# Optimization experiments

Measured on AMD Instinct MI355X. Metric: run time of the kernel, lower is better.

## Reference

```python
import jax, jax.numpy as jnp
import numpy as np

B, S, D, H = 2, 2048, 1024, 16
HD = D // H  # 64


def setup_inputs() -> dict:
    key = jax.random.key(0)
    ks = jax.random.split(key, 9)
    sd = 1.0 / np.sqrt(D)  # torch Linear default init scale (uniform, but normal ok for ref)
    return {
        "x": jax.random.normal(ks[0], (B, S, D), dtype=jnp.float32),
        # torch Linear weight is [out, in]; stack per head -> [H, HD, D]
        "Wq": jax.random.normal(ks[1], (H, HD, D), dtype=jnp.float32) * sd,
        "bq": jax.random.normal(ks[2], (H, HD), dtype=jnp.float32) * sd,
        "Wk": jax.random.normal(ks[3], (H, HD, D), dtype=jnp.float32) * sd,
        "bk": jax.random.normal(ks[4], (H, HD), dtype=jnp.float32) * sd,
        "Wv": jax.random.normal(ks[5], (H, HD, D), dtype=jnp.float32) * sd,
        "bv": jax.random.normal(ks[6], (H, HD), dtype=jnp.float32) * sd,
        "Wp": jax.random.normal(ks[7], (D, D), dtype=jnp.float32) * sd,
        "bp": jax.random.normal(ks[8], (D,), dtype=jnp.float32) * sd,
    }


def reference(x, Wq, bq, Wk, bk, Wv, bv, Wp, bp):
    # Per-head QKV projections, batched over heads: [B,S,D] x [H,HD,D] -> [B,H,S,HD]
    q = jnp.einsum("bsd,hed->bhse", x, Wq) + bq[None, :, None, :]
    k = jnp.einsum("bsd,hed->bhse", x, Wk) + bk[None, :, None, :]
    v = jnp.einsum("bsd,hed->bhse", x, Wv) + bv[None, :, None, :]
    scale = 1.0 / np.sqrt(HD)
    scores = jnp.einsum("bhse,bhte->bhst", q, k) * scale  # [B,H,S,S]
    attn = jax.nn.softmax(scores, axis=-1)
    out = jnp.einsum("bhst,bhte->bhse", attn, v)  # [B,H,S,HD]
    # concat heads along last dim (head-major order matches torch.cat over heads)
    out = out.transpose(0, 2, 1, 3).reshape(x.shape[0], x.shape[1], -1)  # [B,S,D]
    return out @ Wp.T + bp
```

## Files before the change

kernel.cpp:

```cpp
#include <hip/hip_runtime.h>
#include <hip/hip_bf16.h>
#include <stdint.h>

#define B_  2
#define S_  2048
#define D_  1024
#define H_  16
#define HD_ 64
#define M_  (B_*S_)
#define BH_ (B_*H_)

typedef __bf16 bf16;
typedef bf16  bf16x8 __attribute__((ext_vector_type(8)));
typedef bf16  bf16x4 __attribute__((ext_vector_type(4)));
typedef bf16  bf16x2 __attribute__((ext_vector_type(2)));
typedef float f32x4  __attribute__((ext_vector_type(4)));

#define SCALE_LOG2E 0.18033688011112042f
#define MFIX_LOG2E  23.083120654223415f

__device__ __forceinline__ f32x4 mfma16(bf16x8 a, bf16x8 b, f32x4 c) {
    return __builtin_amdgcn_mfma_f32_16x16x32_bf16(a, b, c, 0, 0, 0);
}
__device__ __forceinline__ float fexp2(float x) {
    return __builtin_amdgcn_exp2f(x);
}

__device__ __forceinline__ void gload_lds16(const bf16* g, bf16* l) {
    auto* gp = reinterpret_cast<__attribute__((address_space(1))) uint32_t*>(
        reinterpret_cast<uintptr_t>(const_cast<bf16*>(g)));
    auto* lp = reinterpret_cast<__attribute__((address_space(3))) uint32_t*>(
        reinterpret_cast<uintptr_t>(l));
    __builtin_amdgcn_global_load_lds(gp, lp, 16, 0, 0);
}

__global__ __launch_bounds__(256) void k_convert(
        const float* __restrict__ x,
        const float* __restrict__ wq, const float* __restrict__ wk,
        const float* __restrict__ wv, const float* __restrict__ wp,
        bf16* __restrict__ xb,
        bf16* __restrict__ wqb, bf16* __restrict__ wkb,
        bf16* __restrict__ wvb, bf16* __restrict__ wpb) {
    const int y = blockIdx.y;
    const float* src = (y == 0) ? x : (y == 1) ? wq : (y == 2) ? wk
                     : (y == 3) ? wv : wp;
    bf16* dst        = (y == 0) ? xb : (y == 1) ? wqb : (y == 2) ? wkb
                     : (y == 3) ? wvb : wpb;
    const int reps = (y == 0) ? 4 : 1;
    const int idx = blockIdx.x * 256 + threadIdx.x;
    for (int rep = 0; rep < reps; ++rep) {
        const size_t e = (size_t)rep * (1u << 20) + (size_t)idx * 4;
        const float4 f = *(const float4*)(src + e);
        bf16x4 o;
        o[0] = (bf16)f.x; o[1] = (bf16)f.y; o[2] = (bf16)f.z; o[3] = (bf16)f.w;
        *(bf16x4*)(dst + e) = o;
    }
}

__global__ __launch_bounds__(256) void k_gemm_qkv(
        const bf16* __restrict__ x,
        const bf16* __restrict__ Wq, const bf16* __restrict__ Wk, const bf16* __restrict__ Wv,
        const float* __restrict__ bq, const float* __restrict__ bk, const float* __restrict__ bv,
        bf16* __restrict__ q, bf16* __restrict__ k, bf16* __restrict__ vt) {
    const int z = blockIdx.z;
    const bf16* A   = x;
    const bf16* Bt  = (z == 0) ? Wq : (z == 1) ? Wk : Wv;
    const float* bias = (z == 0) ? bq : (z == 1) ? bk : bv;
    bf16* C         = (z == 0) ? q  : (z == 1) ? k  : vt;

    __shared__ bf16 As[128*32];
    __shared__ bf16 Bs[128*32];
    const int K = D_;
    const int tid = threadIdx.x;
    const int w  = tid >> 6, L = tid & 63;
    const int lr = L & 15,  lq = L >> 4;
    const int tileM = blockIdx.y * 128, tileN = blockIdx.x * 128;
    const int wm = (w >> 1) * 64, wn = (w & 1) * 64;

    const f32x4 fzero = {0.f, 0.f, 0.f, 0.f};
    f32x4 acc[4][4];
#pragma unroll
    for (int i = 0; i < 4; ++i)
#pragma unroll
        for (int j = 0; j < 4; ++j) acc[i][j] = fzero;

    const int srow   = L >> 2;
    const int schunk = (L & 3) ^ (srow & 3);
    const bf16* ag = A  + (size_t)(tileM + w*32 + srow) * K + schunk*8;
    const bf16* bg = Bt + (size_t)(tileN + w*32 + srow) * K + schunk*8;
    bf16* asd = &As[(w*32)*32];
    bf16* bsd = &Bs[(w*32)*32];
    const int sw = lr & 3;

    for (int kt = 0; kt < K; kt += 32) {
        __syncthreads();
        gload_lds16(ag + kt,          asd);
        gload_lds16(ag + kt + 16*K,   asd + 16*32);
        gload_lds16(bg + kt,          bsd);
        gload_lds16(bg + kt + 16*K,   bsd + 16*32);
        __syncthreads();

        bf16x8 af[4], bfr[4];
#pragma unroll
        for (int i = 0; i < 4; ++i)
            af[i]  = *(const bf16x8*)&As[(wm + i*16 + lr)*32 + ((lq ^ sw) * 8)];
#pragma unroll
        for (int j = 0; j < 4; ++j)
            bfr[j] = *(const bf16x8*)&Bs[(wn + j*16 + lr)*32 + ((lq ^ sw) * 8)];
#pragma unroll
        for (int i = 0; i < 4; ++i)
#pragma unroll
            for (int j = 0; j < 4; ++j)
                acc[i][j] = mfma16(af[i], bfr[j], acc[i][j]);
    }

#pragma unroll
    for (int i = 0; i < 4; ++i) {
#pragma unroll
        for (int j = 0; j < 4; ++j) {
            const int m0 = tileM + wm + i*16 + lq*4;
            const int n  = tileN + wn + j*16 + lr;
            const int h = n >> 6, e = n & 63;
            if (z != 2) {
#pragma unroll
                for (int r = 0; r < 4; ++r) {
                    const int m = m0 + r;
                    const int b = m >> 11, s = m & (S_ - 1);
                    C[((size_t)((b*H_ + h)*S_ + s) << 6) + e] =
                        (bf16)(acc[i][j][r] + bias[n]);
                }
            } else {
                const int b = m0 >> 11, s0 = m0 & (S_ - 1);
                const int s0p = (s0 & ~31) | (lq*8) | ((i & 1)*4);
                const float bn = bias[n];
                bf16x4 t4;
#pragma unroll
                for (int r = 0; r < 4; ++r) t4[r] = (bf16)(acc[i][j][r] + bn);
                *(bf16x4*)&C[(((size_t)(b*H_ + h)*HD_ + e) << 11) + s0p] = t4;
            }
        }
    }
}

__global__ __launch_bounds__(256, 4) void k_gemm_proj(
        const bf16* __restrict__ A, const bf16* __restrict__ Bt,
        const float* __restrict__ bias, float* __restrict__ C) {
    __shared__ bf16 As[64*32];
    __shared__ bf16 Bs[128*32];
    const int K = D_;
    const int tid = threadIdx.x;
    const int w  = tid >> 6, L = tid & 63;
    const int lr = L & 15,  lq = L >> 4;
    const int tileM = blockIdx.y * 64, tileN = blockIdx.x * 128;
    const int wm = (w >> 1) * 32, wn = (w & 1) * 64;

    const f32x4 fzero = {0.f, 0.f, 0.f, 0.f};
    f32x4 acc[2][4];
#pragma unroll
    for (int i = 0; i < 2; ++i)
#pragma unroll
        for (int j = 0; j < 4; ++j) acc[i][j] = fzero;

    const int srow   = L >> 2;
    const int schunk = (L & 3) ^ (srow & 3);
    const bf16* ag = A  + (size_t)(tileM + w*16 + srow) * K + schunk*8;
    const bf16* bg = Bt + (size_t)(tileN + w*16 + srow) * K + schunk*8;
    bf16* asd = &As[(w*16)*32];
    bf16* bsd = &Bs[(w*16)*32];
    const int sw = lr & 3;

    for (int kt = 0; kt < K; kt += 32) {
        __syncthreads();
        gload_lds16(ag + kt,          asd);
        gload_lds16(bg + kt,          bsd);
        gload_lds16(bg + kt + 64*K,   bsd + 64*32);
        __syncthreads();

        bf16x8 af[2], bfr[4];
#pragma unroll
        for (int i = 0; i < 2; ++i)
            af[i]  = *(const bf16x8*)&As[(wm + i*16 + lr)*32 + ((lq ^ sw) * 8)];
#pragma unroll
        for (int j = 0; j < 4; ++j)
            bfr[j] = *(const bf16x8*)&Bs[(wn + j*16 + lr)*32 + ((lq ^ sw) * 8)];
#pragma unroll
        for (int i = 0; i < 2; ++i)
#pragma unroll
            for (int j = 0; j < 4; ++j)
                acc[i][j] = mfma16(af[i], bfr[j], acc[i][j]);
    }

#pragma unroll
    for (int i = 0; i < 2; ++i) {
#pragma unroll
        for (int j = 0; j < 4; ++j) {
#pragma unroll
            for (int r = 0; r < 4; ++r) {
                const int m = tileM + wm + i*16 + lq*4 + r;
                const int n = tileN + wn + j*16 + lr;
                C[(size_t)m * D_ + n] = acc[i][j][r] + bias[n];
            }
        }
    }
}

__global__ __launch_bounds__(256, 2) void k_attn(const bf16* __restrict__ Q,
                                                 const bf16* __restrict__ Kg,
                                                 const bf16* __restrict__ Vt,
                                                 bf16* __restrict__ O) {
    __shared__ bf16 Ks[2][64*64];
    __shared__ bf16 Vs[2][64*64];
    const int tid = threadIdx.x;
    const int w  = tid >> 6, L = tid & 63;
    const int lr = L & 15,  lq = L >> 4;
    const int bh = blockIdx.y;
    const int q0 = blockIdx.x * 128 + w * 32;
    const size_t base = (size_t)bh * S_ * HD_;
    const bf16* qp = Q  + base;
    const bf16* kp = Kg + base;
    const bf16* vp = Vt + base;

    bf16x8 qf[2][2];
#pragma unroll
    for (int h2 = 0; h2 < 2; ++h2) {
        qf[h2][0] = *(const bf16x8*)&qp[(q0 + h2*16 + lr)*HD_ + lq*8];
        qf[h2][1] = *(const bf16x8*)&qp[(q0 + h2*16 + lr)*HD_ + 32 + lq*8];
    }

    const int rbase = (w & 1) * 32;
    const int srow  = L >> 3;
    const int gchunk = (L & 7) ^ srow;

    const int c0 = ((lq ^ (lr & 7))) * 8;
    const int c1 = ((lq ^ (lr & 7)) ^ 4) * 8;

    const f32x4 fzero = {0.f, 0.f, 0.f, 0.f};
    float l_lane[2] = {0.f, 0.f};
    f32x4 o_acc[2][4];
#pragma unroll
    for (int h2 = 0; h2 < 2; ++h2)
#pragma unroll
        for (int eb = 0; eb < 4; ++eb) o_acc[h2][eb] = fzero;

    if (w < 2) {
#pragma unroll
        for (int i = 0; i < 4; ++i)
            gload_lds16(kp + (size_t)(rbase + i*8 + srow)*HD_ + gchunk*8,
                        &Ks[0][(rbase + i*8)*HD_]);
    } else {
#pragma unroll
        for (int i = 0; i < 4; ++i)
            gload_lds16(vp + (size_t)(rbase + i*8 + srow)*S_ + gchunk*8,
                        &Vs[0][(rbase + i*8)*HD_]);
    }
    __syncthreads();

    for (int it = 0; it < S_/64; ++it) {
        const int cur = it & 1, nxt = cur ^ 1;
        if (it + 1 < S_/64) {
            const int t1 = (it + 1) * 64;
            if (w < 2) {
#pragma unroll
                for (int i = 0; i < 4; ++i)
                    gload_lds16(kp + (size_t)(t1 + rbase + i*8 + srow)*HD_ + gchunk*8,
                                &Ks[nxt][(rbase + i*8)*HD_]);
            } else {
#pragma unroll
                for (int i = 0; i < 4; ++i)
                    gload_lds16(vp + (size_t)(rbase + i*8 + srow)*S_ + t1 + gchunk*8,
                                &Vs[nxt][(rbase + i*8)*HD_]);
            }
        }

        bf16x4 d4[2][4];
#pragma unroll
        for (int j = 0; j < 4; ++j) {
            const bf16x8 kf0 = *(const bf16x8*)&Ks[cur][(j*16 + lr)*HD_ + c0];
            const bf16x8 kf1 = *(const bf16x8*)&Ks[cur][(j*16 + lr)*HD_ + c1];
#pragma unroll
            for (int h2 = 0; h2 < 2; ++h2) {
                f32x4 z = fzero;
                z = mfma16(kf0, qf[h2][0], z);
                z = mfma16(kf1, qf[h2][1], z);
                bf16x4 t4;
                float ls = 0.f;
#pragma unroll
                for (int r = 0; r < 4; ++r) {
                    const float pv = fexp2(
                        __builtin_fmaf(z[r], SCALE_LOG2E, -MFIX_LOG2E));
                    ls += pv;
                    t4[r] = (bf16)pv;
                }
                l_lane[h2] += ls;
                d4[h2][j] = t4;
            }
        }

        bf16x8 pb[2][2];
#pragma unroll
        for (int h2 = 0; h2 < 2; ++h2) {
#pragma unroll
            for (int kh = 0; kh < 2; ++kh) {
                union { bf16x4 h[2]; bf16x8 v; } u;
                u.h[0] = d4[h2][2*kh + 0];
                u.h[1] = d4[h2][2*kh + 1];
                pb[h2][kh] = u.v;
            }
        }

#pragma unroll
        for (int eb = 0; eb < 4; ++eb) {
            const bf16x8 vb0 = *(const bf16x8*)&Vs[cur][(eb*16 + lr)*HD_ + c0];
            const bf16x8 vb1 = *(const bf16x8*)&Vs[cur][(eb*16 + lr)*HD_ + c1];
#pragma unroll
            for (int h2 = 0; h2 < 2; ++h2) {
                o_acc[h2][eb] = mfma16(vb0, pb[h2][0], o_acc[h2][eb]);
                o_acc[h2][eb] = mfma16(vb1, pb[h2][1], o_acc[h2][eb]);
            }
        }

        if (it + 1 < S_/64) __syncthreads();
    }

    const int b = bh >> 4, h = bh & 15;
#pragma unroll
    for (int h2 = 0; h2 < 2; ++h2) {
        float l = l_lane[h2];
        l += __shfl_xor(l, 16);
        l += __shfl_xor(l, 32);
        const float inv = 1.f / l;
        const size_t obase = ((size_t)(b*S_ + q0 + h2*16 + lr))*D_ + h*64;
#pragma unroll
        for (int eb = 0; eb < 4; ++eb)
#pragma unroll
            for (int b2 = 0; b2 < 2; ++b2) {
                bf16x2 t2 = { (bf16)(o_acc[h2][eb][2*b2]   * inv),
                              (bf16)(o_acc[h2][eb][2*b2+1] * inv) };
                *(bf16x2*)&O[obase + eb*16 + lq*4 + 2*b2] = t2;
            }
    }
}

extern "C" void kernel_launch(void* const* d_in, const int* in_sizes, int n_in,
                              void* d_out, int out_size, void* d_ws, size_t ws_size,
                              hipStream_t stream) {
    const float* x  = (const float*)d_in[0];
    const float* Wq = (const float*)d_in[1];
    const float* bq = (const float*)d_in[2];
    const float* Wk = (const float*)d_in[3];
    const float* bk = (const float*)d_in[4];
    const float* Wv = (const float*)d_in[5];
    const float* bv = (const float*)d_in[6];
    const float* Wp = (const float*)d_in[7];
    const float* bp = (const float*)d_in[8];
    float* out = (float*)d_out;

    const size_t NE = (size_t)B_ * H_ * S_ * HD_;
    const size_t NW = (size_t)D_ * D_;
    bf16* xb  = (bf16*)d_ws;
    bf16* wqb = xb + NE;
    bf16* wkb = wqb + NW;
    bf16* wvb = wkb + NW;
    bf16* wpb = wvb + NW;
    bf16* q_ws  = wpb + NW;
    bf16* k_ws  = q_ws + NE;
    bf16* vt_ws = k_ws + NE;
    bf16* a_ws  = xb;

    k_convert<<<dim3(1024, 5), 256, 0, stream>>>(x, Wq, Wk, Wv, Wp,
                                                 xb, wqb, wkb, wvb, wpb);
    k_gemm_qkv<<<dim3(D_/128, M_/128, 3), 256, 0, stream>>>(
        xb, wqb, wkb, wvb, bq, bk, bv, q_ws, k_ws, vt_ws);
    k_attn<<<dim3(S_/128, BH_), 256, 0, stream>>>(q_ws, k_ws, vt_ws, a_ws);
    k_gemm_proj<<<dim3(D_/128, M_/64), 256, 0, stream>>>(a_ws, wpb, bp, out);
}
```

Before: 190.7 us.

## Triple-buffer K/V tiles in attention with vmcnt-based waits and one barrier

Changes the attention kernel's K/V shared-memory staging from double to triple buffering. It prefetches two tiles ahead and replaces the full __syncthreads with a partial s_waitcnt vmcnt plus a single s_barrier per iteration. The aim is to hide global-to-LDS load latency and drop one barrier per step. In exchange, LDS use per block grows from 32KB to 48KB, which may limit occupancy under launch_bounds(256,2). The hand-placed vmcnt wait also has to match the number of outstanding loads exactly.

```diff
diff --git a/kernel.cpp b/kernel.cpp
--- a/kernel.cpp
+++ b/kernel.cpp
@@ -208,8 +208,8 @@
                                                  const bf16* __restrict__ Kg,
                                                  const bf16* __restrict__ Vt,
                                                  bf16* __restrict__ O) {
-    __shared__ bf16 Ks[2][64*64];
-    __shared__ bf16 Vs[2][64*64];
+    __shared__ bf16 Ks[3][64*64];
+    __shared__ bf16 Vs[3][64*64];
     const int tid = threadIdx.x;
     const int w  = tid >> 6, L = tid & 63;
     const int lr = L & 15,  lq = L >> 4;
@@ -242,33 +242,45 @@
 #pragma unroll
         for (int eb = 0; eb < 4; ++eb) o_acc[h2][eb] = fzero;
 
-    if (w < 2) {
-#pragma unroll
-        for (int i = 0; i < 4; ++i)
-            gload_lds16(kp + (size_t)(rbase + i*8 + srow)*HD_ + gchunk*8,
-                        &Ks[0][(rbase + i*8)*HD_]);
-    } else {
-#pragma unroll
-        for (int i = 0; i < 4; ++i)
-            gload_lds16(vp + (size_t)(rbase + i*8 + srow)*S_ + gchunk*8,
-                        &Vs[0][(rbase + i*8)*HD_]);
-    }
-    __syncthreads();
-
+#pragma unroll
+    for (int t = 0; t < 2; ++t) {
+        const int tb = t * 64;
+        if (w < 2) {
+#pragma unroll
+            for (int i = 0; i < 4; ++i)
+                gload_lds16(kp + (size_t)(tb + rbase + i*8 + srow)*HD_ + gchunk*8,
+                            &Ks[t][(rbase + i*8)*HD_]);
+        } else {
+#pragma unroll
+            for (int i = 0; i < 4; ++i)
+                gload_lds16(vp + (size_t)(rbase + i*8 + srow)*S_ + tb + gchunk*8,
+                            &Vs[t][(rbase + i*8)*HD_]);
+        }
+    }
+
+    int cur = 0;
     for (int it = 0; it < S_/64; ++it) {
-        const int cur = it & 1, nxt = cur ^ 1;
         if (it + 1 < S_/64) {
-            const int t1 = (it + 1) * 64;
+            asm volatile("s_waitcnt vmcnt(4)" ::: "memory");
+        } else {
+            asm volatile("s_waitcnt vmcnt(0)" ::: "memory");
+        }
+        __builtin_amdgcn_s_barrier();
+        __builtin_amdgcn_sched_barrier(0);
+
+        if (it + 2 < S_/64) {
+            const int pbuf = (cur >= 1) ? cur - 1 : cur + 2;
+            const int t2 = (it + 2) * 64;
             if (w < 2) {
 #pragma unroll
                 for (int i = 0; i < 4; ++i)
-                    gload_lds16(kp + (size_t)(t1 + rbase + i*8 + srow)*HD_ + gchunk*8,
-                                &Ks[nxt][(rbase + i*8)*HD_]);
+                    gload_lds16(kp + (size_t)(t2 + rbase + i*8 + srow)*HD_ + gchunk*8,
+                                &Ks[pbuf][(rbase + i*8)*HD_]);
             } else {
 #pragma unroll
                 for (int i = 0; i < 4; ++i)
-                    gload_lds16(vp + (size_t)(rbase + i*8 + srow)*S_ + t1 + gchunk*8,
-                                &Vs[nxt][(rbase + i*8)*HD_]);
+                    gload_lds16(vp + (size_t)(rbase + i*8 + srow)*S_ + t2 + gchunk*8,
+                                &Vs[pbuf][(rbase + i*8)*HD_]);
             }
         }
 
@@ -319,7 +331,7 @@
             }
         }
 
-        if (it + 1 < S_/64) __syncthreads();
+        cur = (cur == 2) ? 0 : cur + 1;
     }
 
     const int b = bh >> 4, h = bh & 15;
```

New measurement: 190.0 us. No clear change (-0.4%).
